# Optimization experiments

Hardware: AMD Instinct MI355X
Metric: run time of the kernel (lower is better)

## Reference

```python
import jax, jax.numpy as jnp
import numpy as np

DIM = 2048
HEADS = 16
HEAD_DIM = 128
B = 2
T = 2048


def _rope_as_in_source(x):
    # x: (b, h, t, d). FAITHFUL to the source bug: RotaryEmbedding uses
    # x.shape[1] (the HEADS axis, since it is called after transpose) as the
    # 'sequence' index, so rotation angle depends on head index and is
    # broadcast over the true sequence axis.
    n = x.shape[1]  # == heads
    d = x.shape[-1]
    inv_freq = 1.0 / (10000.0 ** (jnp.arange(0, d, 2, dtype=jnp.float32) / d))
    freqs = jnp.arange(n, dtype=jnp.float32)[:, None] * inv_freq[None, :]  # (h, d/2)
    cos = jnp.cos(freqs)[None, :, None, :]  # (1, h, 1, d/2)
    sin = jnp.sin(freqs)[None, :, None, :]
    x1 = x[..., 0::2]
    x2 = x[..., 1::2]
    out = jnp.stack([x1 * cos - x2 * sin, x1 * sin + x2 * cos], axis=-1)
    return out.reshape(x.shape)


def setup_inputs() -> dict:
    key = jax.random.key(0)
    ks = jax.random.split(key, 9)
    s_in = 1.0 / np.sqrt(DIM)
    hd = HEADS * HEAD_DIM
    s_o = 1.0 / np.sqrt(hd)
    return {
        "x": jax.random.normal(ks[0], (B, T, DIM), dtype=jnp.float32),
        "Wq": jax.random.normal(ks[1], (DIM, hd), dtype=jnp.float32) * s_in,
        "bq": jnp.zeros((hd,), dtype=jnp.float32),
        "Wk": jax.random.normal(ks[2], (DIM, hd), dtype=jnp.float32) * s_in,
        "bk": jnp.zeros((hd,), dtype=jnp.float32),
        "Wv": jax.random.normal(ks[3], (DIM, hd), dtype=jnp.float32) * s_in,
        "bv": jnp.zeros((hd,), dtype=jnp.float32),
        "Wo": jax.random.normal(ks[4], (hd, DIM), dtype=jnp.float32) * s_o,
        "bo": jnp.zeros((DIM,), dtype=jnp.float32),
    }


def reference(x, Wq, bq, Wk, bk, Wv, bv, Wo, bo):
    b, t, c = x.shape
    q = (x @ Wq + bq).reshape(b, t, HEADS, HEAD_DIM).transpose(0, 2, 1, 3)
    k = (x @ Wk + bk).reshape(b, t, HEADS, HEAD_DIM).transpose(0, 2, 1, 3)
    v = (x @ Wv + bv).reshape(b, t, HEADS, HEAD_DIM).transpose(0, 2, 1, 3)
    q = _rope_as_in_source(q)
    k = _rope_as_in_source(k)
    scale = 1.0 / np.sqrt(HEAD_DIM)
    scores = jnp.einsum("bhqd,bhkd->bhqk", q, k) * scale  # (b,h,t,t)
    attn = jax.nn.softmax(scores, axis=-1)
    out = jnp.einsum("bhqk,bhkd->bhqd", attn, v)  # (b,h,t,d)
    out = out.transpose(0, 2, 1, 3).reshape(b, t, HEADS * HEAD_DIM)
    return out @ Wo + bo
```

## Files before the change

### kernel.cpp

```cpp
#include <hip/hip_runtime.h>

typedef unsigned short ushort_t;
typedef unsigned int uint_t;
typedef __attribute__((ext_vector_type(8))) short short8;
typedef __attribute__((ext_vector_type(4))) float f32x4;
typedef __attribute__((ext_vector_type(4))) unsigned short ushort4_t;
typedef __attribute__((ext_vector_type(4))) unsigned int uint4_t;

__device__ inline ushort_t f2b(float f) {
    unsigned int x = __builtin_bit_cast(unsigned int, f);
    x += 0x7fffu + ((x >> 16) & 1u);
    return (ushort_t)(x >> 16);
}
__device__ inline uint_t cvt_pk_bf16(float lo, float hi) {
    uint_t r;
    asm("v_cvt_pk_bf16_f32 %0, %1, %2" : "=v"(r) : "v"(lo), "v"(hi));
    return r;
}

__device__ inline void gload16(const void* g, void* l) {
    __builtin_amdgcn_global_load_lds(
        (const __attribute__((address_space(1))) void*)g,
        (__attribute__((address_space(3))) void*)l, 16, 0, 0);
}

__global__ __launch_bounds__(256)
void cast_bf16(const float* __restrict__ src, ushort_t* __restrict__ dst) {
    size_t i = ((size_t)blockIdx.x * 256 + threadIdx.x) * 8;
    f32x4 a = *reinterpret_cast<const f32x4*>(src + i);
    f32x4 b = *reinterpret_cast<const f32x4*>(src + i + 4);
    short8 v;
#pragma unroll
    for (int j = 0; j < 4; ++j) { v[j] = (short)f2b(a[j]); v[4 + j] = (short)f2b(b[j]); }
    *reinterpret_cast<short8*>(dst + i) = v;
}

__global__ __launch_bounds__(64)
void transp4(const float* __restrict__ s0, const float* __restrict__ s1,
             const float* __restrict__ s2, const float* __restrict__ s3,
             ushort_t* __restrict__ d0, ushort_t* __restrict__ d1,
             ushort_t* __restrict__ d2, ushort_t* __restrict__ d3) {
    const int z = blockIdx.z;
    const float* src = (z == 0) ? s0 : (z == 1) ? s1 : (z == 2) ? s2 : s3;
    ushort_t* dst = (z == 0) ? d0 : (z == 1) ? d1 : (z == 2) ? d2 : d3;
    const int R = 2048, C = 2048;
    int r0 = blockIdx.x * 64 + ((threadIdx.x >> 3) << 3);
    int c0 = blockIdx.y * 64 + ((threadIdx.x & 7) << 3);
    ushort_t v[8][8];
#pragma unroll
    for (int i = 0; i < 8; ++i) {
        const float* p = src + (size_t)(r0 + i) * C + c0;
        f32x4 a = *reinterpret_cast<const f32x4*>(p);
        f32x4 b = *reinterpret_cast<const f32x4*>(p + 4);
#pragma unroll
        for (int j = 0; j < 4; ++j) { v[i][j] = f2b(a[j]); v[i][4 + j] = f2b(b[j]); }
    }
#pragma unroll
    for (int c = 0; c < 8; ++c) {
        short8 w;
#pragma unroll
        for (int i = 0; i < 8; ++i) w[i] = (short)v[i][c];
        *reinterpret_cast<short8*>(dst + (size_t)(c0 + c) * R + r0) = w;
    }
}

__global__ __launch_bounds__(256)
void gemm_qkv(const ushort_t* __restrict__ A,
              const ushort_t* __restrict__ Btq, const ushort_t* __restrict__ Btk,
              const ushort_t* __restrict__ Btv,
              const float* __restrict__ bqp, const float* __restrict__ bkp,
              const float* __restrict__ bvp,
              ushort_t* __restrict__ Qb, ushort_t* __restrict__ Kb,
              ushort_t* __restrict__ Vtb, float qsc) {
    const int z = blockIdx.z;
    const ushort_t* Bt = (z == 0) ? Btq : (z == 1) ? Btk : Btv;
    const float* bias = (z == 0) ? bqp : (z == 1) ? bkp : bvp;
    ushort_t* C = (z == 0) ? Qb : (z == 1) ? Kb : Vtb;
    const float oscale = (z == 0) ? qsc : 1.0f;
    const int K = 2048;
    __shared__ __align__(16) ushort_t As[128 * 64];
    __shared__ __align__(16) ushort_t Bs[128 * 64];
    const int tid = threadIdx.x, lane = tid & 63, wid = tid >> 6;
    const int l15 = lane & 15, g = lane >> 4;
    const int wr = wid >> 1, wc = wid & 1;
    const int m0 = blockIdx.y * 128, n0 = blockIdx.x * 128;
    f32x4 acc[4][4] = {};
    for (int k0 = 0; k0 < K; k0 += 64) {
#pragma unroll
        for (int is = 0; is < 4; ++is) {
            int c = is * 256 + tid;
            int row = c >> 3, sub = c & 7;
            int ks = (sub ^ (row & 7)) << 3;
            char* ldst = (char*)As + (size_t)(is * 256 + wid * 64) * 16;
            gload16(A + (size_t)(m0 + row) * K + k0 + ks, ldst);
            char* ldstB = (char*)Bs + (size_t)(is * 256 + wid * 64) * 16;
            gload16(Bt + (size_t)(n0 + row) * K + k0 + ks, ldstB);
        }
        __syncthreads();
#pragma unroll
        for (int kk = 0; kk < 2; ++kk) {
            short8 af[4], bf[4];
#pragma unroll
            for (int i = 0; i < 4; ++i) {
                int ra = wr * 64 + i * 16 + l15;
                af[i] = *reinterpret_cast<const short8*>(
                    (const char*)As + ra * 128 + (((4 * kk + g) ^ (ra & 7)) << 4));
                int rb = wc * 64 + i * 16 + l15;
                bf[i] = *reinterpret_cast<const short8*>(
                    (const char*)Bs + rb * 128 + (((4 * kk + g) ^ (rb & 7)) << 4));
            }
#pragma unroll
            for (int i = 0; i < 4; ++i)
#pragma unroll
                for (int j = 0; j < 4; ++j)
                    acc[i][j] = __builtin_amdgcn_mfma_f32_16x16x32_bf16(af[i], bf[j], acc[i][j], 0, 0, 0);
        }
        __syncthreads();
    }
#pragma unroll
    for (int j = 0; j < 4; ++j) {
        int n = n0 + wc * 64 + j * 16 + l15;
        float bj = bias[n];
        float sn = 0.f, cs = 1.f, sgn = 0.f;
        if (z < 2) {
            int d = n & 127, h = (n >> 7) & 15;
            float inv = expf(-(float)(d >> 1) * (9.210340371976184f / 64.0f));
            sincosf((float)h * inv, &sn, &cs);
            sgn = (d & 1) ? sn : -sn;
        }
#pragma unroll
        for (int i = 0; i < 4; ++i) {
            int mbase = m0 + wr * 64 + i * 16 + g * 4;
            if (z == 2) {
                int d = n & 127, hh = n >> 7;
                int b_ = mbase >> 11, t0 = mbase & 2047;
                ushort4_t w;
#pragma unroll
                for (int r = 0; r < 4; ++r) w[r] = f2b(acc[i][j][r] + bj);
                *reinterpret_cast<ushort4_t*>(
                    C + (((size_t)(b_ * 16 + hh) * 128 + d) * 2048 + t0)) = w;
            } else {
#pragma unroll
                for (int r = 0; r < 4; ++r) {
                    int m = mbase + r;
                    float v = acc[i][j][r] + bj;
                    float p = __shfl_xor(v, 1, 64);
                    v = fmaf(p, sgn, v * cs);
                    v *= oscale;
                    size_t addr = ((size_t)((m >> 11) * 16 + (n >> 7)) * 2048 + (m & 2047)) * 128 + (n & 127);
                    C[addr] = f2b(v);
                }
            }
        }
    }
}

__global__ __launch_bounds__(256)
void gemm_out(const ushort_t* __restrict__ A, const ushort_t* __restrict__ Bt,
              const float* __restrict__ bias, float* __restrict__ C,
              int M, int N, int K) {
    __shared__ __align__(16) ushort_t As[128 * 64];
    __shared__ __align__(16) ushort_t Bs[128 * 64];
    const int tid = threadIdx.x, lane = tid & 63, wid = tid >> 6;
    const int l15 = lane & 15, g = lane >> 4;
    const int wr = wid >> 1, wc = wid & 1;
    const int m0 = blockIdx.y * 128, n0 = blockIdx.x * 128;
    f32x4 acc[4][4] = {};
    for (int k0 = 0; k0 < K; k0 += 64) {
#pragma unroll
        for (int is = 0; is < 4; ++is) {
            int c = is * 256 + tid;
            int row = c >> 3, sub = c & 7;
            int ks = (sub ^ (row & 7)) << 3;
            char* ldst = (char*)As + (size_t)(is * 256 + wid * 64) * 16;
            gload16(A + (size_t)(m0 + row) * K + k0 + ks, ldst);
            char* ldstB = (char*)Bs + (size_t)(is * 256 + wid * 64) * 16;
            gload16(Bt + (size_t)(n0 + row) * K + k0 + ks, ldstB);
        }
        __syncthreads();
#pragma unroll
        for (int kk = 0; kk < 2; ++kk) {
            short8 af[4], bf[4];
#pragma unroll
            for (int i = 0; i < 4; ++i) {
                int ra = wr * 64 + i * 16 + l15;
                af[i] = *reinterpret_cast<const short8*>(
                    (const char*)As + ra * 128 + (((4 * kk + g) ^ (ra & 7)) << 4));
                int rb = wc * 64 + i * 16 + l15;
                bf[i] = *reinterpret_cast<const short8*>(
                    (const char*)Bs + rb * 128 + (((4 * kk + g) ^ (rb & 7)) << 4));
            }
#pragma unroll
            for (int i = 0; i < 4; ++i)
#pragma unroll
                for (int j = 0; j < 4; ++j)
                    acc[i][j] = __builtin_amdgcn_mfma_f32_16x16x32_bf16(af[i], bf[j], acc[i][j], 0, 0, 0);
        }
        __syncthreads();
    }
#pragma unroll
    for (int j = 0; j < 4; ++j) {
        int n = n0 + wc * 64 + j * 16 + l15;
        float bj = bias[n];
#pragma unroll
        for (int i = 0; i < 4; ++i) {
            int mbase = m0 + wr * 64 + i * 16 + g * 4;
#pragma unroll
            for (int r = 0; r < 4; ++r)
                C[(size_t)(mbase + r) * N + n] = acc[i][j][r] + bj;
        }
    }
}

__global__ __launch_bounds__(512)
void fattn(const ushort_t* __restrict__ Q, const ushort_t* __restrict__ K,
           const ushort_t* __restrict__ Vt, ushort_t* __restrict__ O) {
    __shared__ __align__(16) ushort_t Ks[2][64 * 128];
    __shared__ __align__(16) ushort_t Vs[2][128 * 64];
    const int tid = threadIdx.x, lane = tid & 63, wid = tid >> 6;
    const int l15 = lane & 15, g = lane >> 4;
    const int h = blockIdx.y, b = blockIdx.z;
    const size_t base = ((size_t)b * 16 + h) * (2048 * 128);
    const int q0 = blockIdx.x * 128 + wid * 16;
    short8 qf[4];
#pragma unroll
    for (int c = 0; c < 4; ++c)
        qf[c] = *reinterpret_cast<const short8*>(Q + base + (size_t)(q0 + l15) * 128 + c * 32 + g * 8);
    f32x4 oacc[8] = {};
    f32x4 oaccL = {};
    float m_r = -__builtin_inff();
    short8 ones;
#pragma unroll
    for (int j = 0; j < 8; ++j) ones[j] = (short)0x3F80;
    const int addrA = ((32 * (g & 1)) + l15) << 2;
    const int addrB = addrA + 64;
    const bool hi = (lane & 32) != 0;

    auto stage = [&](int kv0, int bsel) {
#pragma unroll
        for (int is = 0; is < 2; ++is) {
            {
                int c = is * 512 + tid;
                int row = c >> 4, sub = c & 15;
                int dsrc = (sub ^ (row & 7)) << 3;
                gload16(K + base + (size_t)(kv0 + row) * 128 + dsrc,
                        (char*)Ks[bsel] + (size_t)c * 16);
            }
            {
                int c = is * 512 + tid;
                int row = c >> 3, sub = c & 7;
                int tsrc = (sub ^ (row & 7)) << 3;
                gload16(Vt + base + (size_t)row * 2048 + kv0 + tsrc,
                        (char*)Vs[bsel] + (size_t)c * 16);
            }
        }
    };

    stage(0, 0);
    asm volatile("s_waitcnt vmcnt(0)" ::: "memory");
    __builtin_amdgcn_s_barrier();

    for (int it = 0; it < 32; ++it) {
        const int cur = it & 1;
        if (it < 31) stage((it + 1) << 6, cur ^ 1);
        f32x4 s[4] = {};
        __builtin_amdgcn_s_setprio(1);
#pragma unroll
        for (int nt = 0; nt < 4; ++nt) {
            int kvr = nt * 16 + l15;
#pragma unroll
            for (int c = 0; c < 4; ++c) {
                short8 kf = *reinterpret_cast<const short8*>(
                    (const char*)Ks[cur] + kvr * 256 + (((4 * c + g) ^ (kvr & 7)) << 4));
                s[nt] = __builtin_amdgcn_mfma_f32_16x16x32_bf16(kf, qf[c], s[nt], 0, 0, 0);
            }
        }
        __builtin_amdgcn_s_setprio(0);
        float pm = fmaxf(fmaxf(fmaxf(s[0][0], s[0][1]), fmaxf(s[0][2], s[0][3])),
                         fmaxf(fmaxf(s[1][0], s[1][1]), fmaxf(s[1][2], s[1][3])));
        pm = fmaxf(pm, fmaxf(fmaxf(fmaxf(s[2][0], s[2][1]), fmaxf(s[2][2], s[2][3])),
                             fmaxf(fmaxf(s[3][0], s[3][1]), fmaxf(s[3][2], s[3][3]))));
        pm = fmaxf(pm, __shfl_xor(pm, 16, 64));
        pm = fmaxf(pm, __shfl_xor(pm, 32, 64));
        if (!__all(pm <= m_r + 5.0f)) {
            float mn = fmaxf(m_r, pm);
            float fac = exp2f(m_r - mn);
            m_r = mn;
#pragma unroll
            for (int r = 0; r < 4; ++r) oaccL[r] *= fac;
#pragma unroll
            for (int nt2 = 0; nt2 < 8; ++nt2)
#pragma unroll
                for (int r = 0; r < 4; ++r) oacc[nt2][r] *= fac;
        }
        uint_t W[4][2];
#pragma unroll
        for (int nt = 0; nt < 4; ++nt) {
            float p0 = exp2f(s[nt][0] - m_r);
            float p1 = exp2f(s[nt][1] - m_r);
            float p2 = exp2f(s[nt][2] - m_r);
            float p3 = exp2f(s[nt][3] - m_r);
            W[nt][0] = cvt_pk_bf16(p0, p1);
            W[nt][1] = cvt_pk_bf16(p2, p3);
        }
        __builtin_amdgcn_s_setprio(1);
#pragma unroll
        for (int ks = 0; ks < 2; ++ks) {
            uint_t xa, xb, w0, w1, w2, w3;
            xa = (uint_t)__builtin_amdgcn_ds_bpermute(addrA, (int)W[2 * ks][0]);
            xb = (uint_t)__builtin_amdgcn_ds_bpermute(addrA, (int)W[2 * ks + 1][0]);
            w0 = hi ? xb : xa;
            xa = (uint_t)__builtin_amdgcn_ds_bpermute(addrA, (int)W[2 * ks][1]);
            xb = (uint_t)__builtin_amdgcn_ds_bpermute(addrA, (int)W[2 * ks + 1][1]);
            w1 = hi ? xb : xa;
            xa = (uint_t)__builtin_amdgcn_ds_bpermute(addrB, (int)W[2 * ks][0]);
            xb = (uint_t)__builtin_amdgcn_ds_bpermute(addrB, (int)W[2 * ks + 1][0]);
            w2 = hi ? xb : xa;
            xa = (uint_t)__builtin_amdgcn_ds_bpermute(addrB, (int)W[2 * ks][1]);
            xb = (uint_t)__builtin_amdgcn_ds_bpermute(addrB, (int)W[2 * ks + 1][1]);
            w3 = hi ? xb : xa;
            uint4_t wv; wv[0] = w0; wv[1] = w1; wv[2] = w2; wv[3] = w3;
            short8 pb = __builtin_bit_cast(short8, wv);
            oaccL = __builtin_amdgcn_mfma_f32_16x16x32_bf16(ones, pb, oaccL, 0, 0, 0);
#pragma unroll
            for (int nt2 = 0; nt2 < 8; ++nt2) {
                int dr = nt2 * 16 + l15;
                short8 vb = *reinterpret_cast<const short8*>(
                    (const char*)Vs[cur] + dr * 128 + (((ks * 4 + g) ^ (dr & 7)) << 4));
                oacc[nt2] = __builtin_amdgcn_mfma_f32_16x16x32_bf16(vb, pb, oacc[nt2], 0, 0, 0);
            }
        }
        __builtin_amdgcn_s_setprio(0);
        asm volatile("s_waitcnt vmcnt(0)" ::: "memory");
        __builtin_amdgcn_s_barrier();
    }
    float inv = 1.f / oaccL[0];
    const size_t orow = ((size_t)b * 2048 + q0 + l15) * 2048 + (size_t)h * 128;
#pragma unroll
    for (int nt2 = 0; nt2 < 8; ++nt2) {
        ushort4_t w;
#pragma unroll
        for (int r = 0; r < 4; ++r) w[r] = f2b(oacc[nt2][r] * inv);
        *reinterpret_cast<ushort4_t*>(O + orow + nt2 * 16 + g * 4) = w;
    }
}

extern "C" void kernel_launch(void* const* d_in, const int* in_sizes, int n_in,
                              void* d_out, int out_size, void* d_ws, size_t ws_size,
                              hipStream_t stream) {
    const float* x  = (const float*)d_in[0];
    const float* Wq = (const float*)d_in[1];
    const float* bq = (const float*)d_in[2];
    const float* Wk = (const float*)d_in[3];
    const float* bk = (const float*)d_in[4];
    const float* Wv = (const float*)d_in[5];
    const float* bv = (const float*)d_in[6];
    const float* Wo = (const float*)d_in[7];
    const float* bo = (const float*)d_in[8];
    float* out = (float*)d_out;
    ushort_t* ws  = (ushort_t*)d_ws;

    const size_t WSZ = 2048ull * 2048;
    const size_t TSZ = 2ull * 16 * 2048 * 128;
    ushort_t* xb  = ws;
    ushort_t* Wtq = xb + TSZ;
    ushort_t* Wtk = Wtq + WSZ;
    ushort_t* Wtv = Wtk + WSZ;
    ushort_t* Wto = Wtv + WSZ;
    ushort_t* Qb  = Wto + WSZ;
    ushort_t* Kb  = Qb + TSZ;
    ushort_t* Vtb = Kb + TSZ;
    ushort_t* Sb  = Vtb + TSZ;

    const float QSC = 0.08838834764831845f * 1.4426950408889634f;

    cast_bf16<<<dim3(4096), 256, 0, stream>>>(x, xb);
    transp4<<<dim3(32, 32, 4), 64, 0, stream>>>(Wq, Wk, Wv, Wo, Wtq, Wtk, Wtv, Wto);

    gemm_qkv<<<dim3(16, 32, 3), 256, 0, stream>>>(xb, Wtq, Wtk, Wtv, bq, bk, bv,
                                                  Qb, Kb, Vtb, QSC);

    fattn<<<dim3(16, 16, 2), 512, 0, stream>>>(Qb, Kb, Vtb, Sb);

    gemm_out<<<dim3(16, 32), 256, 0, stream>>>(Sb, Wto, bo, out, 4096, 2048, 2048);
}
```

Baseline: 315.0 us.

## Replace bpermute shuffles with permlane32 swap via permuted K rows; split QKV GEMM

The attention kernel now loads K rows in a permuted order, so the probability fragments only need a v_permlane32_swap to reach the layout the PV MFMA expects. This replaces eight ds_bpermute LDS-crossbar ops and selects per step with two register swaps. Separately, the fused QKV GEMM launch becomes three template-specialized launches, which removes runtime branching on the z index. The trade-off is three smaller launches with less parallelism each in place of one larger one.

```diff
diff --git a/kernel.cpp b/kernel.cpp
--- a/kernel.cpp
+++ b/kernel.cpp
@@ -64,19 +64,10 @@
     }
 }
 
+template <int MODE>
 __global__ __launch_bounds__(256)
-void gemm_qkv(const ushort_t* __restrict__ A,
-              const ushort_t* __restrict__ Btq, const ushort_t* __restrict__ Btk,
-              const ushort_t* __restrict__ Btv,
-              const float* __restrict__ bqp, const float* __restrict__ bkp,
-              const float* __restrict__ bvp,
-              ushort_t* __restrict__ Qb, ushort_t* __restrict__ Kb,
-              ushort_t* __restrict__ Vtb, float qsc) {
-    const int z = blockIdx.z;
-    const ushort_t* Bt = (z == 0) ? Btq : (z == 1) ? Btk : Btv;
-    const float* bias = (z == 0) ? bqp : (z == 1) ? bkp : bvp;
-    ushort_t* C = (z == 0) ? Qb : (z == 1) ? Kb : Vtb;
-    const float oscale = (z == 0) ? qsc : 1.0f;
+void gemm_qkv(const ushort_t* __restrict__ A, const ushort_t* __restrict__ Bt,
+              const float* __restrict__ bias, ushort_t* __restrict__ C, float oscale) {
     const int K = 2048;
     __shared__ __align__(16) ushort_t As[128 * 64];
     __shared__ __align__(16) ushort_t Bs[128 * 64];
@@ -122,7 +113,7 @@
         int n = n0 + wc * 64 + j * 16 + l15;
         float bj = bias[n];
         float sn = 0.f, cs = 1.f, sgn = 0.f;
-        if (z < 2) {
+        if (MODE == 0) {
             int d = n & 127, h = (n >> 7) & 15;
             float inv = expf(-(float)(d >> 1) * (9.210340371976184f / 64.0f));
             sincosf((float)h * inv, &sn, &cs);
@@ -131,7 +122,7 @@
 #pragma unroll
         for (int i = 0; i < 4; ++i) {
             int mbase = m0 + wr * 64 + i * 16 + g * 4;
-            if (z == 2) {
+            if (MODE == 2) {
                 int d = n & 127, hh = n >> 7;
                 int b_ = mbase >> 11, t0 = mbase & 2047;
                 ushort4_t w;
@@ -222,6 +213,8 @@
     const int h = blockIdx.y, b = blockIdx.z;
     const size_t base = ((size_t)b * 16 + h) * (2048 * 128);
     const int q0 = blockIdx.x * 128 + wid * 16;
+    const int q2 = l15 >> 2;
+    const int sig = ((q2 == 1) ? 2 : (q2 == 2) ? 1 : q2) * 4 + (l15 & 3);
     short8 qf[4];
 #pragma unroll
     for (int c = 0; c < 4; ++c)
@@ -232,9 +225,6 @@
     short8 ones;
 #pragma unroll
     for (int j = 0; j < 8; ++j) ones[j] = (short)0x3F80;
-    const int addrA = ((32 * (g & 1)) + l15) << 2;
-    const int addrB = addrA + 64;
-    const bool hi = (lane & 32) != 0;
 
     auto stage = [&](int kv0, int bsel) {
 #pragma unroll
@@ -267,11 +257,11 @@
         __builtin_amdgcn_s_setprio(1);
 #pragma unroll
         for (int nt = 0; nt < 4; ++nt) {
-            int kvr = nt * 16 + l15;
+            int kvr = nt * 16 + sig;
 #pragma unroll
             for (int c = 0; c < 4; ++c) {
                 short8 kf = *reinterpret_cast<const short8*>(
-                    (const char*)Ks[cur] + kvr * 256 + (((4 * c + g) ^ (kvr & 7)) << 4));
+                    (const char*)Ks[cur] + kvr * 256 + (((4 * c + g) ^ (sig & 7)) << 4));
                 s[nt] = __builtin_amdgcn_mfma_f32_16x16x32_bf16(kf, qf[c], s[nt], 0, 0, 0);
             }
         }
@@ -306,20 +296,11 @@
         __builtin_amdgcn_s_setprio(1);
 #pragma unroll
         for (int ks = 0; ks < 2; ++ks) {
-            uint_t xa, xb, w0, w1, w2, w3;
-            xa = (uint_t)__builtin_amdgcn_ds_bpermute(addrA, (int)W[2 * ks][0]);
-            xb = (uint_t)__builtin_amdgcn_ds_bpermute(addrA, (int)W[2 * ks + 1][0]);
-            w0 = hi ? xb : xa;
-            xa = (uint_t)__builtin_amdgcn_ds_bpermute(addrA, (int)W[2 * ks][1]);
-            xb = (uint_t)__builtin_amdgcn_ds_bpermute(addrA, (int)W[2 * ks + 1][1]);
-            w1 = hi ? xb : xa;
-            xa = (uint_t)__builtin_amdgcn_ds_bpermute(addrB, (int)W[2 * ks][0]);
-            xb = (uint_t)__builtin_amdgcn_ds_bpermute(addrB, (int)W[2 * ks + 1][0]);
-            w2 = hi ? xb : xa;
-            xa = (uint_t)__builtin_amdgcn_ds_bpermute(addrB, (int)W[2 * ks][1]);
-            xb = (uint_t)__builtin_amdgcn_ds_bpermute(addrB, (int)W[2 * ks + 1][1]);
-            w3 = hi ? xb : xa;
-            uint4_t wv; wv[0] = w0; wv[1] = w1; wv[2] = w2; wv[3] = w3;
+            uint_t A0 = W[2 * ks][0], A1 = W[2 * ks][1];
+            uint_t B0 = W[2 * ks + 1][0], B1 = W[2 * ks + 1][1];
+            asm("v_permlane32_swap_b32 %0, %1" : "+v"(A0), "+v"(B0));
+            asm("v_permlane32_swap_b32 %0, %1" : "+v"(A1), "+v"(B1));
+            uint4_t wv; wv[0] = A0; wv[1] = A1; wv[2] = B0; wv[3] = B1;
             short8 pb = __builtin_bit_cast(short8, wv);
             oaccL = __builtin_amdgcn_mfma_f32_16x16x32_bf16(ones, pb, oaccL, 0, 0, 0);
 #pragma unroll
@@ -377,8 +358,9 @@
     cast_bf16<<<dim3(4096), 256, 0, stream>>>(x, xb);
     transp4<<<dim3(32, 32, 4), 64, 0, stream>>>(Wq, Wk, Wv, Wo, Wtq, Wtk, Wtv, Wto);
 
-    gemm_qkv<<<dim3(16, 32, 3), 256, 0, stream>>>(xb, Wtq, Wtk, Wtv, bq, bk, bv,
-                                                  Qb, Kb, Vtb, QSC);
+    gemm_qkv<0><<<dim3(16, 32), 256, 0, stream>>>(xb, Wtq, bq, Qb, QSC);
+    gemm_qkv<0><<<dim3(16, 32), 256, 0, stream>>>(xb, Wtk, bk, Kb, 1.0f);
+    gemm_qkv<2><<<dim3(16, 32), 256, 0, stream>>>(xb, Wtv, bv, Vtb, 1.0f);
 
     fattn<<<dim3(16, 16, 2), 512, 0, stream>>>(Qb, Kb, Vtb, Sb);
 
```

New measurement: 307.0 us. -2.6%, faster.
